# Optimization experiments

Hardware: AMD Instinct MI355X
Metric: run time of the kernel (lower is better)

Reference implementation:

```python
import jax, jax.numpy as jnp
import numpy as np
from jax import lax

# ---- static config (matches init_kwargs) ----
B, D, H, HD, MLP = 64, 768, 12, 64, 3072
DEPTH = 11                     # trunk blocks; block 12 is used (twice) as b1/b2
IMG_H, IMG_W, P, S = 256, 128, 16, 12
NY, NX = (IMG_H - P) // S + 1, (IMG_W - P) // S + 1   # 21, 10
NP = NY * NX                   # 210 patches
N = NP + 1                     # +CLS = 211 tokens
NUM_CIDS = 8
SCALE = HD ** -0.5
SIE = 3.0                      # sie_xishu
SHIFT, GROUPS, DIV = 5, 2, 4
EPS = 1e-6
_PNAMES = ["ln1_g", "ln1_b", "qkv_w", "qkv_b", "proj_w", "proj_b",
           "ln2_g", "ln2_b", "fc1_w", "fc1_b", "fc2_w", "fc2_b"]


def layernorm(x, g, b):
    m = jnp.mean(x, -1, keepdims=True)
    v = jnp.mean(jnp.square(x - m), -1, keepdims=True)
    return (x - m) * lax.rsqrt(v + EPS) * g + b


def block(x, p):
    """Pre-norm ViT block: manual attention (q@k.T softmax @v) + GELU MLP."""
    ln1g, ln1b, qkvw, qkvb, projw, projb, ln2g, ln2b, fc1w, fc1b, fc2w, fc2b = p
    Bn, Nn = x.shape[0], x.shape[1]
    h = layernorm(x, ln1g, ln1b)
    qkv = (h @ qkvw + qkvb).reshape(Bn, Nn, 3, H, HD)
    q, k, v = qkv[:, :, 0], qkv[:, :, 1], qkv[:, :, 2]           # [B,N,H,HD]
    attn = jax.nn.softmax(jnp.einsum('bnhd,bmhd->bhnm', q * SCALE, k), axis=-1)
    o = jnp.einsum('bhnm,bmhd->bnhd', attn, v).reshape(Bn, Nn, D)
    x = x + o @ projw + projb
    h = layernorm(x, ln2g, ln2b)
    return x + jax.nn.gelu(h @ fc1w + fc1b, approximate=False) @ fc2w + fc2b


def _block_params(k, lead=()):
    ks = jax.random.split(k, 4)
    z = lambda s: jnp.zeros(lead + s, jnp.float32)
    o = lambda s: jnp.ones(lead + s, jnp.float32)
    r = lambda kk, s, fan: jax.random.normal(kk, lead + s, jnp.float32) * (fan ** -0.5)
    return dict(ln1_g=o((D,)), ln1_b=z((D,)),
                qkv_w=r(ks[0], (D, 3 * D), D), qkv_b=z((3 * D,)),
                proj_w=r(ks[1], (D, D), D), proj_b=z((D,)),
                ln2_g=o((D,)), ln2_b=z((D,)),
                fc1_w=r(ks[2], (D, MLP), D), fc1_b=z((MLP,)),
                fc2_w=r(ks[3], (MLP, D), MLP), fc2_b=z((D,)))


def setup_inputs() -> dict:
    key = jax.random.key(0)
    k = jax.random.split(key, 8)
    inp = {
        "x": jax.random.normal(k[0], (B, 3, IMG_H, IMG_W), jnp.float32),
        "cids": jax.random.randint(k[1], (B,), 0, NUM_CIDS),
        "conv_w": jax.random.normal(k[2], (D, 3, P, P), jnp.float32) * np.float32(np.sqrt(2.0 / (P * P * D))),
        "conv_b": jnp.zeros((D,), jnp.float32),
        "cls_token": jax.random.normal(k[3], (1, 1, D), jnp.float32) * 0.02,
        "pos_embed": jax.random.normal(k[4], (1, N, D), jnp.float32) * 0.02,
        "sie_embed": jax.random.normal(k[5], (NUM_CIDS, 1, D), jnp.float32) * 0.02,
    }
    for name, arr in _block_params(k[6], (DEPTH,)).items():
        inp["blk_" + name] = arr
    for pre, kk in (("b1_", jax.random.fold_in(key, 101)), ("b2_", jax.random.fold_in(key, 102))):
        for name, arr in _block_params(kk).items():
            inp[pre + name] = arr
        inp[pre + "norm_g"] = jnp.ones((D,), jnp.float32)
        inp[pre + "norm_b"] = jnp.zeros((D,), jnp.float32)
    return inp


def reference(x, cids, conv_w, conv_b, cls_token, pos_embed, sie_embed,
              blk_ln1_g, blk_ln1_b, blk_qkv_w, blk_qkv_b, blk_proj_w, blk_proj_b,
              blk_ln2_g, blk_ln2_b, blk_fc1_w, blk_fc1_b, blk_fc2_w, blk_fc2_b,
              b1_ln1_g, b1_ln1_b, b1_qkv_w, b1_qkv_b, b1_proj_w, b1_proj_b,
              b1_ln2_g, b1_ln2_b, b1_fc1_w, b1_fc1_b, b1_fc2_w, b1_fc2_b,
              b1_norm_g, b1_norm_b,
              b2_ln1_g, b2_ln1_b, b2_qkv_w, b2_qkv_b, b2_proj_w, b2_proj_b,
              b2_ln2_g, b2_ln2_b, b2_fc1_w, b2_fc1_b, b2_fc2_w, b2_fc2_b,
              b2_norm_g, b2_norm_b):
    Bn = x.shape[0]
    # overlapping patch embed: Conv2d(3->768, k=16, s=12), flatten, transpose
    y = lax.conv_general_dilated(x, conv_w, (S, S), 'VALID',
                                 dimension_numbers=('NCHW', 'OIHW', 'NCHW'))
    y = (y + conv_b[None, :, None, None]).reshape(Bn, D, NP).transpose(0, 2, 1)
    t = jnp.concatenate([jnp.broadcast_to(cls_token, (Bn, 1, D)), y], axis=1)
    t = t + pos_embed + SIE * sie_embed[cids]   # SIE camera embedding
    # 11 trunk blocks via scan over stacked params
    stk = (blk_ln1_g, blk_ln1_b, blk_qkv_w, blk_qkv_b, blk_proj_w, blk_proj_b,
           blk_ln2_g, blk_ln2_b, blk_fc1_w, blk_fc1_b, blk_fc2_w, blk_fc2_b)
    t = lax.scan(lambda c, p: (block(c, p), None), t, stk)[0]
    # global branch: b1 = block12 + final norm, take CLS
    b1p = (b1_ln1_g, b1_ln1_b, b1_qkv_w, b1_qkv_b, b1_proj_w, b1_proj_b,
           b1_ln2_g, b1_ln2_b, b1_fc1_w, b1_fc1_b, b1_fc2_w, b1_fc2_b)
    f0 = layernorm(block(t, b1p), b1_norm_g, b1_norm_b)[:, 0]
    # shuffle_unit(t, shift=5, group=2, begin=1) -> jigsaw rearranged patches [B,210,D]
    xs = jnp.concatenate([t[:, SHIFT:], t[:, 1:SHIFT]], axis=1)
    xs = xs.reshape(Bn, GROUPS, -1, D).transpose(0, 2, 1, 3).reshape(Bn, -1, D)
    token = t[:, 0:1]
    pl = NP // DIV                                   # 52
    b2p = (b2_ln1_g, b2_ln1_b, b2_qkv_w, b2_qkv_b, b2_proj_w, b2_proj_b,
           b2_ln2_g, b2_ln2_b, b2_fc1_w, b2_fc1_b, b2_fc2_w, b2_fc2_b)
    feats = [f0]
    for i in range(DIV):
        seg = jnp.concatenate([token, xs[:, i * pl:(i + 1) * pl]], axis=1)   # [B,53,D]
        feats.append(layernorm(block(seg, b2p), b2_norm_g, b2_norm_b)[:, 0])
    # eval output with neck_feat='before': necks pass features through;
    # concat global + local/divide_length -> [B, 5*768]
    return jnp.concatenate([feats[0]] + [f / DIV for f in feats[1:]], axis=1)
```

## Files before the change

kernel.cpp:

```cpp
#include <hip/hip_runtime.h>
#include <hip/hip_bf16.h>
#include <cstdint>
#include <cstddef>
#include <math.h>

using bf16 = __hip_bfloat16;
typedef __bf16 bf16x8 __attribute__((ext_vector_type(8)));
typedef float f32x4 __attribute__((ext_vector_type(4)));

static constexpr int NHEAD = 12;
static constexpr int NTOK  = 211;
static constexpr int DEPTH = 11;

static __device__ __forceinline__ void gload_lds16(const bf16* g, bf16* lds) {
  __builtin_amdgcn_global_load_lds(
      (const __attribute__((address_space(1))) uint32_t*)g,
      (__attribute__((address_space(3))) uint32_t*)lds,
      16, 0, 0);
}

__device__ __forceinline__ float gelu_f(float x) {
  float u = x * (0.7978845608f + 0.0356774081f * x * x);
  float t = 1.f - 2.f / (__expf(2.f * u) + 1.f);
  return 0.5f * x * (1.f + t);
}

static __device__ __forceinline__ unsigned short bf16_bits(float x) {
  return __builtin_bit_cast(unsigned short, __float2bfloat16(x));
}

template <bool GELU, bool RES, typename CT>
__global__ __launch_bounds__(256) void gemm_db(
    const bf16* __restrict__ A, const bf16* __restrict__ Bt,
    const float* __restrict__ bias, const float* __restrict__ res,
    CT* __restrict__ C, int M, int N, int K, int gn, int sA, int sR, int sC)
{
  __shared__ bf16 sb[2][8192];

  const int tid = threadIdx.x;
  const int w = tid >> 6, l = tid & 63;
  const int lr = l & 15, lg = l >> 4;
  const int wr = (w >> 1) * 64, wc = (w & 1) * 64;

  const int nwg = gridDim.x, lin = blockIdx.x;
  const int q = nwg >> 3, r = nwg & 7;
  const int xcd = lin & 7, pos = lin >> 3;
  const int wg = (xcd < r ? xcd * (q + 1) : r * (q + 1) + (xcd - r) * q) + pos;
  const int bm0 = (wg / gn) * 128, bn0 = (wg % gn) * 128;

  f32x4 acc[4][4];
#pragma unroll
  for (int i = 0; i < 4; ++i)
#pragma unroll
    for (int j = 0; j < 4; ++j) acc[i][j] = f32x4{0.f, 0.f, 0.f, 0.f};

  size_t aof[2], bof[2]; int dst[2];
#pragma unroll
  for (int j = 0; j < 2; ++j) {
    const int c = j * 256 + tid;
    const int row = c >> 2;
    const int ch = (c & 3) ^ ((row >> 1) & 3);
    int ar = bm0 + row; if (ar >= M) ar = M - 1;
    aof[j] = (size_t)ar * sA + ch * 8;
    bof[j] = (size_t)(bn0 + row) * K + ch * 8;
    dst[j] = c * 8;
  }

  const int nt = K >> 5;

  auto stage = [&](int t) {
    bf16* s = sb[t & 1];
    const size_t ko = (size_t)t * 32;
    gload_lds16(A + aof[0] + ko, s + dst[0]);
    gload_lds16(A + aof[1] + ko, s + dst[1]);
    gload_lds16(Bt + bof[0] + ko, s + 4096 + dst[0]);
    gload_lds16(Bt + bof[1] + ko, s + 4096 + dst[1]);
  };

  stage(0);
  __syncthreads();

  const int swz = (lg ^ ((lr >> 1) & 3)) * 8;

  for (int t = 0; t < nt; ++t) {
    if (t + 1 < nt) stage(t + 1);
    const bf16* As = sb[t & 1];
    const bf16* Bs = As + 4096;
    bf16x8 af[4], bv[4];
#pragma unroll
    for (int mi = 0; mi < 4; ++mi)
      af[mi] = *(const bf16x8*)(As + (wr + mi * 16 + lr) * 32 + swz);
#pragma unroll
    for (int ni = 0; ni < 4; ++ni)
      bv[ni] = *(const bf16x8*)(Bs + (wc + ni * 16 + lr) * 32 + swz);
#pragma unroll
    for (int mi = 0; mi < 4; ++mi)
#pragma unroll
      for (int ni = 0; ni < 4; ++ni)
        acc[mi][ni] = __builtin_amdgcn_mfma_f32_16x16x32_bf16(af[mi], bv[ni], acc[mi][ni], 0, 0, 0);
    __syncthreads();
  }

  if constexpr (sizeof(CT) == 2) {
    char* lb = (char*)sb;
#pragma unroll
    for (int mi = 0; mi < 4; ++mi) {
#pragma unroll
      for (int ni = 0; ni < 4; ++ni) {
        const int cloc = wc + ni * 16 + lr;
        const float bvl = bias[bn0 + cloc];
#pragma unroll
        for (int r2 = 0; r2 < 4; ++r2) {
          const int rowl = wr + mi * 16 + lg * 4 + r2;
          float v = acc[mi][ni][r2] + bvl;
          if constexpr (GELU) v = gelu_f(v);
          *(unsigned short*)(lb + rowl * 256 + ((cloc * 2) ^ (((rowl >> 1) & 6) << 4))) =
              bf16_bits(v);
        }
      }
    }
    __syncthreads();
#pragma unroll
    for (int j = 0; j < 8; ++j) {
      const int flat = j * 256 + tid;
      const int row = flat >> 4, ch = flat & 15;
      const int grow = bm0 + row;
      if (grow < M) {
        const f32x4 v = *(const f32x4*)(lb + row * 256 + ((ch * 16) ^ (((row >> 1) & 6) << 4)));
        *(f32x4*)((char*)C + ((size_t)grow * sC + bn0 + ch * 8) * 2) = v;
      }
    }
  } else {
#pragma unroll
    for (int mi = 0; mi < 4; ++mi) {
#pragma unroll
      for (int ni = 0; ni < 4; ++ni) {
        const int col = bn0 + wc + ni * 16 + lr;
        const float bvl = bias[col];
#pragma unroll
        for (int r2 = 0; r2 < 4; ++r2) {
          const int row = bm0 + wr + mi * 16 + lg * 4 + r2;
          if (row < M) {
            float v = acc[mi][ni][r2] + bvl;
            if constexpr (GELU) v = gelu_f(v);
            if constexpr (RES) v += res[(size_t)row * sR + col];
            C[(size_t)row * sC + col] = v;
          }
        }
      }
    }
  }
}

__global__ __launch_bounds__(256) void vtrans_kernel(
    const bf16* __restrict__ qkv, bf16* __restrict__ vT, int ntok, int pad)
{
  __shared__ unsigned short t[224 * 65];
  const int bb = blockIdx.x, h = blockIdx.y;
  const unsigned short* src = (const unsigned short*)qkv + (size_t)bb * ntok * 2304 + 1536 + h * 64;
  for (int idx = threadIdx.x; idx < ntok * 64; idx += 256) {
    int tok = idx >> 6, d = idx & 63;
    t[tok * 65 + d] = src[(size_t)tok * 2304 + d];
  }
  __syncthreads();
  unsigned short* dst = (unsigned short*)vT + (size_t)(bb * 12 + h) * 64 * pad;
  for (int idx = threadIdx.x; idx < 64 * ntok; idx += 256) {
    int d = idx / ntok, tok = idx - d * ntok;
    dst[(size_t)d * pad + tok] = t[tok * 65 + d];
  }
}

template <int NKF, bool ONLY0>
__global__ __launch_bounds__(256) void attn_kernel(
    const bf16* __restrict__ qkv, const bf16* __restrict__ vT,
    bf16* __restrict__ ao, int ntok, int pad)
{
  constexpr int NPAD = NKF * 16;
  __shared__ bf16 Pl[4][16][NPAD];
  const int bb = blockIdx.x;
  const int h = blockIdx.y;
  const int tid = threadIdx.x;
  const int w = tid >> 6, l = tid & 63;
  const int lr = l & 15, lg = l >> 4;
  if (ONLY0 && w > 0) return;
  const __bf16* base = reinterpret_cast<const __bf16*>(qkv) + (size_t)bb * ntok * 2304 + h * 64;
  const __bf16* vt = reinterpret_cast<const __bf16*>(vT) + (size_t)(bb * 12 + h) * 64 * pad;

  for (int qt = w; qt < (ONLY0 ? 1 : NKF); qt += 4) {
    int qrow = qt * 16 + lr; if (qrow >= ntok) qrow = ntok - 1;
    const __bf16* qp = base + (size_t)qrow * 2304 + lg * 8;
    const bf16x8 qf0 = *reinterpret_cast<const bf16x8*>(qp);
    const bf16x8 qf1 = *reinterpret_cast<const bf16x8*>(qp + 32);

    f32x4 s[NKF];
#pragma unroll
    for (int kf = 0; kf < NKF; ++kf) {
      int krow = kf * 16 + lr; if (krow >= ntok) krow = ntok - 1;
      const __bf16* kp = base + (size_t)krow * 2304 + 768 + lg * 8;
      f32x4 a = f32x4{0.f, 0.f, 0.f, 0.f};
      a = __builtin_amdgcn_mfma_f32_16x16x32_bf16(qf0, *reinterpret_cast<const bf16x8*>(kp), a, 0, 0, 0);
      a = __builtin_amdgcn_mfma_f32_16x16x32_bf16(qf1, *reinterpret_cast<const bf16x8*>(kp + 32), a, 0, 0, 0);
      s[kf] = a;
    }

    float rs[4];
#pragma unroll
    for (int r = 0; r < 4; ++r) {
      float mx = -1e30f;
#pragma unroll
      for (int kf = 0; kf < NKF; ++kf)
        if (kf * 16 + lr < ntok) mx = fmaxf(mx, s[kf][r]);
#pragma unroll
      for (int d = 1; d < 16; d <<= 1) mx = fmaxf(mx, __shfl_xor(mx, d));
      float sum = 0.f;
#pragma unroll
      for (int kf = 0; kf < NKF; ++kf) {
        float p = 0.f;
        if (kf * 16 + lr < ntok) p = __expf((s[kf][r] - mx) * 0.125f);
        sum += p;
        Pl[w][lg * 4 + r][kf * 16 + lr] = __float2bfloat16(p);
      }
#pragma unroll
      for (int d = 1; d < 16; d <<= 1) sum += __shfl_xor(sum, d);
      rs[r] = sum;
    }
    __builtin_amdgcn_s_waitcnt(0);

    f32x4 o[4];
#pragma unroll
    for (int ni = 0; ni < 4; ++ni) o[ni] = f32x4{0.f, 0.f, 0.f, 0.f};
#pragma unroll
    for (int ks = 0; ks < NPAD / 32; ++ks) {
      const bf16x8 pa = *reinterpret_cast<const bf16x8*>(&Pl[w][lr][ks * 32 + lg * 8]);
#pragma unroll
      for (int ni = 0; ni < 4; ++ni) {
        const bf16x8 vb = *reinterpret_cast<const bf16x8*>(
            vt + (size_t)(ni * 16 + lr) * pad + ks * 32 + lg * 8);
        o[ni] = __builtin_amdgcn_mfma_f32_16x16x32_bf16(pa, vb, o[ni], 0, 0, 0);
      }
    }
#pragma unroll
    for (int ni = 0; ni < 4; ++ni)
#pragma unroll
      for (int r = 0; r < 4; ++r) {
        int qq = qt * 16 + lg * 4 + r;
        if (qq < (ONLY0 ? 1 : ntok)) {
          float val = o[ni][r] / rs[r];
          ao[((size_t)bb * ntok + qq) * 768 + h * 64 + ni * 16 + lr] = __float2bfloat16(val);
        }
      }
  }
}

__global__ __launch_bounds__(256) void ln_kernel(
    const float* __restrict__ x, const float* __restrict__ g, const float* __restrict__ b,
    bf16* __restrict__ out, int Mrows)
{
  int row = blockIdx.x * 4 + (threadIdx.x >> 6);
  if (row >= Mrows) return;
  int l = threadIdx.x & 63;
  const float4* xr = reinterpret_cast<const float4*>(x + (size_t)row * 768);
  float4 v[3]; float s = 0.f;
#pragma unroll
  for (int i = 0; i < 3; ++i) {
    v[i] = xr[l + i * 64];
    s += v[i].x + v[i].y + v[i].z + v[i].w;
  }
#pragma unroll
  for (int d = 1; d < 64; d <<= 1) s += __shfl_xor(s, d);
  float mean = s * (1.f / 768.f);
  float s2 = 0.f;
#pragma unroll
  for (int i = 0; i < 3; ++i) {
    float a0 = v[i].x - mean, a1 = v[i].y - mean, a2 = v[i].z - mean, a3 = v[i].w - mean;
    s2 += a0 * a0 + a1 * a1 + a2 * a2 + a3 * a3;
  }
#pragma unroll
  for (int d = 1; d < 64; d <<= 1) s2 += __shfl_xor(s2, d);
  float rstd = rsqrtf(s2 * (1.f / 768.f) + 1e-6f);
  const float4* g4 = reinterpret_cast<const float4*>(g);
  const float4* b4 = reinterpret_cast<const float4*>(b);
  unsigned short* orow = reinterpret_cast<unsigned short*>(out + (size_t)row * 768);
#pragma unroll
  for (int i = 0; i < 3; ++i) {
    float4 gg = g4[l + i * 64], bb = b4[l + i * 64];
    ushort4 pk;
    pk.x = bf16_bits((v[i].x - mean) * rstd * gg.x + bb.x);
    pk.y = bf16_bits((v[i].y - mean) * rstd * gg.y + bb.y);
    pk.z = bf16_bits((v[i].z - mean) * rstd * gg.z + bb.z);
    pk.w = bf16_bits((v[i].w - mean) * rstd * gg.w + bb.w);
    *reinterpret_cast<ushort4*>(orow + (l + i * 64) * 4) = pk;
  }
}

__global__ __launch_bounds__(256) void ln_head_kernel(
    const float* __restrict__ x, int tokstride, const float* __restrict__ g,
    const float* __restrict__ b, float* __restrict__ out, int nbb, int mode)
{
  int bb = blockIdx.x * 4 + (threadIdx.x >> 6);
  if (bb >= nbb) return;
  int l = threadIdx.x & 63;
  const float* xr = x + (size_t)bb * tokstride * 768;
  float v[12]; float s = 0.f;
#pragma unroll
  for (int i = 0; i < 12; ++i) { v[i] = xr[l + i * 64]; s += v[i]; }
#pragma unroll
  for (int d = 1; d < 64; d <<= 1) s += __shfl_xor(s, d);
  float mean = s * (1.f / 768.f);
  float s2 = 0.f;
#pragma unroll
  for (int i = 0; i < 12; ++i) { float t = v[i] - mean; s2 += t * t; }
#pragma unroll
  for (int d = 1; d < 64; d <<= 1) s2 += __shfl_xor(s2, d);
  float rstd = rsqrtf(s2 * (1.f / 768.f) + 1e-6f);
  float scale = mode ? 0.25f : 1.f;
  int b_ = mode ? (bb & 63) : bb;
  int off = mode ? (1 + (bb >> 6)) * 768 : 0;
  float* orow = out + (size_t)b_ * 3840 + off;
#pragma unroll
  for (int i = 0; i < 12; ++i) {
    orow[l + i * 64] = ((v[i] - mean) * rstd * g[l + i * 64] + b[l + i * 64]) * scale;
  }
}

__global__ __launch_bounds__(256) void transpose4_k(
    const float* __restrict__ w0, const float* __restrict__ w1,
    const float* __restrict__ w2, const float* __restrict__ w3,
    bf16* __restrict__ d0, bf16* __restrict__ d1,
    bf16* __restrict__ d2, bf16* __restrict__ d3)
{
  __shared__ float tile[32][33];
  int id = blockIdx.x;
  const float* in; bf16* out; int R, C, tt;
  if (id < 1728)      { in = w0; out = d0; R = 768;  C = 2304; tt = id; }
  else if (id < 2304) { in = w1; out = d1; R = 768;  C = 768;  tt = id - 1728; }
  else if (id < 4608) { in = w2; out = d2; R = 768;  C = 3072; tt = id - 2304; }
  else                { in = w3; out = d3; R = 3072; C = 768;  tt = id - 4608; }
  const int tc = C >> 5;
  int c0 = (tt % tc) * 32, r0 = (tt / tc) * 32;
  int tx = threadIdx.x & 31, ty = threadIdx.x >> 5;
#pragma unroll
  for (int i = 0; i < 4; ++i) {
    int rr = ty + i * 8;
    tile[rr][tx] = in[(size_t)(r0 + rr) * C + c0 + tx];
  }
  __syncthreads();
#pragma unroll
  for (int i = 0; i < 4; ++i) {
    int c = ty + i * 8;
    out[(size_t)(c0 + c) * R + r0 + tx] = __float2bfloat16(tile[tx][c]);
  }
}

__global__ void cast_kernel(const float* __restrict__ in, bf16* __restrict__ out, int n)
{
  int idx = blockIdx.x * 256 + threadIdx.x;
  if (idx < n) out[idx] = __float2bfloat16(in[idx]);
}

__global__ void im2col_kernel(const float* __restrict__ x, bf16* __restrict__ pm)
{
  int idx = blockIdx.x * 256 + threadIdx.x;
  if (idx >= 13440 * 768) return;
  int k = idx % 768;
  int m = idx / 768;
  int b = m / 210, p = m % 210;
  int py = p / 10, px = p % 10;
  int c = k >> 8, ij = k & 255, i = ij >> 4, j = ij & 15;
  pm[idx] = __float2bfloat16(x[(((size_t)b * 3 + c) * 256 + py * 12 + i) * 128 + px * 12 + j]);
}

__global__ void assemble_kernel(
    const bf16* __restrict__ y, const float* __restrict__ cls, const float* __restrict__ pos,
    const float* __restrict__ sie, const int* __restrict__ cids, float* __restrict__ tA)
{
  int idx = blockIdx.x * 256 + threadIdx.x;
  if (idx >= 13504 * 768) return;
  int d = idx % 768;
  int t = (idx / 768) % 211;
  int b = idx / (768 * 211);
  float v = pos[t * 768 + d] + 3.0f * sie[cids[b] * 768 + d];
  if (t == 0) v += cls[d];
  else v += __bfloat162float(y[((size_t)b * 210 + (t - 1)) * 768 + d]);
  tA[idx] = v;
}

__global__ void gather_kernel(const float* __restrict__ tA, float* __restrict__ tB)
{
  int idx = blockIdx.x * 256 + threadIdx.x;
  if (idx >= 256 * 53 * 768) return;
  int d = idx % 768;
  int jj = (idx / 768) % 53;
  int bb = idx / (768 * 53);
  int i = bb >> 6, b = bb & 63;
  int src;
  if (jj == 0) src = 0;
  else {
    int jx = i * 52 + (jj - 1);
    int mm = (jx & 1) * 105 + (jx >> 1);
    src = (mm < 206) ? (5 + mm) : (1 + (mm - 206));
  }
  tB[idx] = tA[((size_t)b * 211 + src) * 768 + d];
}

struct BlkP {
  const float *ln1_g, *ln1_b, *qkv_w, *qkv_b, *proj_w, *proj_b;
  const float *ln2_g, *ln2_b, *fc1_w, *fc1_b, *fc2_w, *fc2_b;
};

extern "C" void kernel_launch(void* const* d_in, const int* in_sizes, int n_in,
                              void* d_out, int out_size, void* d_ws, size_t ws_size,
                              hipStream_t stream)
{
  (void)in_sizes; (void)n_in; (void)out_size; (void)ws_size;
  const float* xin   = (const float*)d_in[0];
  const int*   cids  = (const int*)  d_in[1];
  const float* convw = (const float*)d_in[2];
  const float* convb = (const float*)d_in[3];
  const float* cls   = (const float*)d_in[4];
  const float* pos   = (const float*)d_in[5];
  const float* sie   = (const float*)d_in[6];
  float* out = (float*)d_out;

  char* ws = (char*)d_ws;
  bf16*  qkvT = (bf16*)(ws + 0);
  bf16*  projT = (bf16*)(ws + 3538944);
  bf16*  fc1T = (bf16*)(ws + 4718592);
  bf16*  fc2T = (bf16*)(ws + 9437184);
  float* tA   = (float*)(ws + 14155776);
  float* tB   = (float*)(ws + 55640064);
  bf16*  hb   = (bf16*)(ws + 97320960);
  bf16*  big  = (bf16*)(ws + 118161408);
  bf16*  ao   = (bf16*)(ws + 201523200);
  bf16*  vTb  = (bf16*)(ws + 222363648);
  char*  sbuf = ws + 118161408 + 73400320;
  float* y0   = (float*)(sbuf);
  bf16*  hb0  = (bf16*)(sbuf + 786432);
  bf16*  big0 = (bf16*)(sbuf + 1179648);
  float* f0b  = (float*)(sbuf + 2752512);

  dim3 blk(256);

  auto apply_block = [&](float* xbuf, const BlkP& p, int nb, int ntok_) {
    const int M = nb * ntok_;
    const int gm = (M + 127) / 128;
    const int pad = (ntok_ == NTOK) ? 224 : 64;
    transpose4_k<<<dim3(6912), blk, 0, stream>>>(
        p.qkv_w, p.proj_w, p.fc1_w, p.fc2_w, qkvT, projT, fc1T, fc2T);
    ln_kernel<<<dim3((M + 3) / 4), blk, 0, stream>>>(xbuf, p.ln1_g, p.ln1_b, hb, M);
    gemm_db<false, false, bf16><<<dim3(gm * 18), blk, 0, stream>>>(
        hb, qkvT, p.qkv_b, nullptr, big, M, 2304, 768, 18, 768, 2304, 2304);
    vtrans_kernel<<<dim3(nb, NHEAD), blk, 0, stream>>>(big, vTb, ntok_, pad);
    attn_kernel<14, false><<<dim3(nb, NHEAD), blk, 0, stream>>>(big, vTb, ao, ntok_, pad);
    gemm_db<false, true, float><<<dim3(gm * 6), blk, 0, stream>>>(
        ao, projT, p.proj_b, xbuf, xbuf, M, 768, 768, 6, 768, 768, 768);
    ln_kernel<<<dim3((M + 3) / 4), blk, 0, stream>>>(xbuf, p.ln2_g, p.ln2_b, hb, M);
    gemm_db<true, false, bf16><<<dim3(gm * 24), blk, 0, stream>>>(
        hb, fc1T, p.fc1_b, nullptr, big, M, 3072, 768, 24, 768, 3072, 3072);
    gemm_db<false, true, float><<<dim3(gm * 6), blk, 0, stream>>>(
        big, fc2T, p.fc2_b, xbuf, xbuf, M, 768, 3072, 6, 3072, 768, 768);
  };

  auto apply_head_block = [&](const float* xsrc, const BlkP& p, int nb, int ntok_,
                              const float* ng, const float* nbias, int mode) {
    const int M = nb * ntok_;
    const int gm = (M + 127) / 128;
    const int gm0 = (nb + 127) / 128;
    const int pad = (ntok_ == NTOK) ? 224 : 64;
    const int ts = ntok_ * 768;
    transpose4_k<<<dim3(6912), blk, 0, stream>>>(
        p.qkv_w, p.proj_w, p.fc1_w, p.fc2_w, qkvT, projT, fc1T, fc2T);
    ln_kernel<<<dim3((M + 3) / 4), blk, 0, stream>>>(xsrc, p.ln1_g, p.ln1_b, hb, M);
    gemm_db<false, false, bf16><<<dim3(gm * 18), blk, 0, stream>>>(
        hb, qkvT, p.qkv_b, nullptr, big, M, 2304, 768, 18, 768, 2304, 2304);
    vtrans_kernel<<<dim3(nb, NHEAD), blk, 0, stream>>>(big, vTb, ntok_, pad);
    if (ntok_ == NTOK)
      attn_kernel<14, true><<<dim3(nb, NHEAD), blk, 0, stream>>>(big, vTb, ao, ntok_, pad);
    else
      attn_kernel<4, true><<<dim3(nb, NHEAD), blk, 0, stream>>>(big, vTb, ao, ntok_, pad);
    gemm_db<false, true, float><<<dim3(gm0 * 6), blk, 0, stream>>>(
        ao, projT, p.proj_b, xsrc, y0, nb, 768, 768, 6, ts, ts, 768);
    ln_kernel<<<dim3((nb + 3) / 4), blk, 0, stream>>>(y0, p.ln2_g, p.ln2_b, hb0, nb);
    gemm_db<true, false, bf16><<<dim3(gm0 * 24), blk, 0, stream>>>(
        hb0, fc1T, p.fc1_b, nullptr, big0, nb, 3072, 768, 24, 768, 3072, 3072);
    gemm_db<false, true, float><<<dim3(gm0 * 6), blk, 0, stream>>>(
        big0, fc2T, p.fc2_b, y0, f0b, nb, 768, 3072, 6, 3072, 768, 768);
    ln_head_kernel<<<dim3((nb + 3) / 4), blk, 0, stream>>>(
        f0b, 1, ng, nbias, out, nb, mode);
  };

  {
    int total = 13440 * 768;
    im2col_kernel<<<dim3((total + 255) / 256), blk, 0, stream>>>(xin, big);
    int nw = 768 * 768;
    cast_kernel<<<dim3((nw + 255) / 256), blk, 0, stream>>>(convw, qkvT, nw);
    gemm_db<false, false, bf16><<<dim3(105 * 6), blk, 0, stream>>>(
        big, qkvT, convb, nullptr, ao, 13440, 768, 768, 6, 768, 768, 768);
    total = 13504 * 768;
    assemble_kernel<<<dim3((total + 255) / 256), blk, 0, stream>>>(ao, cls, pos, sie, cids, tA);
  }

  const float* bp[12];
  for (int i = 0; i < 12; ++i) bp[i] = (const float*)d_in[7 + i];
  for (int dd = 0; dd < DEPTH; ++dd) {
    BlkP p;
    p.ln1_g = bp[0] + dd * 768;                p.ln1_b = bp[1] + dd * 768;
    p.qkv_w = bp[2] + (size_t)dd * 768 * 2304; p.qkv_b = bp[3] + dd * 2304;
    p.proj_w = bp[4] + (size_t)dd * 768 * 768; p.proj_b = bp[5] + dd * 768;
    p.ln2_g = bp[6] + dd * 768;                p.ln2_b = bp[7] + dd * 768;
    p.fc1_w = bp[8] + (size_t)dd * 768 * 3072; p.fc1_b = bp[9] + dd * 3072;
    p.fc2_w = bp[10] + (size_t)dd * 3072 * 768; p.fc2_b = bp[11] + dd * 768;
    apply_block(tA, p, 64, NTOK);
  }

  {
    BlkP p;
    p.ln1_g = (const float*)d_in[19]; p.ln1_b = (const float*)d_in[20];
    p.qkv_w = (const float*)d_in[21]; p.qkv_b = (const float*)d_in[22];
    p.proj_w = (const float*)d_in[23]; p.proj_b = (const float*)d_in[24];
    p.ln2_g = (const float*)d_in[25]; p.ln2_b = (const float*)d_in[26];
    p.fc1_w = (const float*)d_in[27]; p.fc1_b = (const float*)d_in[28];
    p.fc2_w = (const float*)d_in[29]; p.fc2_b = (const float*)d_in[30];
    apply_head_block(tA, p, 64, NTOK,
                     (const float*)d_in[31], (const float*)d_in[32], 0);
  }

  {
    int total = 256 * 53 * 768;
    gather_kernel<<<dim3((total + 255) / 256), blk, 0, stream>>>(tA, tB);
    BlkP p;
    p.ln1_g = (const float*)d_in[33]; p.ln1_b = (const float*)d_in[34];
    p.qkv_w = (const float*)d_in[35]; p.qkv_b = (const float*)d_in[36];
    p.proj_w = (const float*)d_in[37]; p.proj_b = (const float*)d_in[38];
    p.ln2_g = (const float*)d_in[39]; p.ln2_b = (const float*)d_in[40];
    p.fc1_w = (const float*)d_in[41]; p.fc1_b = (const float*)d_in[42];
    p.fc2_w = (const float*)d_in[43]; p.fc2_b = (const float*)d_in[44];
    apply_head_block(tB, p, 256, 53,
                     (const float*)d_in[45], (const float*)d_in[46], 1);
  }
}
```

Baseline: 5.167 ms.

## Switch GEMM to 32x32 MFMA, fuse LN with weight transpose, trim head QKV

```diff
diff --git a/kernel.cpp b/kernel.cpp
--- a/kernel.cpp
+++ b/kernel.cpp
@@ -7,6 +7,7 @@
 using bf16 = __hip_bfloat16;
 typedef __bf16 bf16x8 __attribute__((ext_vector_type(8)));
 typedef float f32x4 __attribute__((ext_vector_type(4)));
+typedef float f32x16 __attribute__((ext_vector_type(16)));
 
 static constexpr int NHEAD = 12;
 static constexpr int NTOK  = 211;
@@ -39,7 +40,7 @@
 
   const int tid = threadIdx.x;
   const int w = tid >> 6, l = tid & 63;
-  const int lr = l & 15, lg = l >> 4;
+  const int l31 = l & 31, lh = l >> 5;
   const int wr = (w >> 1) * 64, wc = (w & 1) * 64;
 
   const int nwg = gridDim.x, lin = blockIdx.x;
@@ -48,11 +49,13 @@
   const int wg = (xcd < r ? xcd * (q + 1) : r * (q + 1) + (xcd - r) * q) + pos;
   const int bm0 = (wg / gn) * 128, bn0 = (wg % gn) * 128;
 
-  f32x4 acc[4][4];
-#pragma unroll
-  for (int i = 0; i < 4; ++i)
-#pragma unroll
-    for (int j = 0; j < 4; ++j) acc[i][j] = f32x4{0.f, 0.f, 0.f, 0.f};
+  f32x16 acc[2][2];
+#pragma unroll
+  for (int i = 0; i < 2; ++i)
+#pragma unroll
+    for (int j = 0; j < 2; ++j)
+#pragma unroll
+      for (int e = 0; e < 16; ++e) acc[i][j][e] = 0.f;
 
   size_t aof[2], bof[2]; int dst[2];
 #pragma unroll
@@ -80,38 +83,50 @@
   stage(0);
   __syncthreads();
 
-  const int swz = (lg ^ ((lr >> 1) & 3)) * 8;
+  const int cswz0 = ((lh)     ^ ((l31 >> 1) & 3)) * 8;
+  const int cswz1 = ((2 + lh) ^ ((l31 >> 1) & 3)) * 8;
 
   for (int t = 0; t < nt; ++t) {
     if (t + 1 < nt) stage(t + 1);
     const bf16* As = sb[t & 1];
     const bf16* Bs = As + 4096;
-    bf16x8 af[4], bv[4];
-#pragma unroll
-    for (int mi = 0; mi < 4; ++mi)
-      af[mi] = *(const bf16x8*)(As + (wr + mi * 16 + lr) * 32 + swz);
-#pragma unroll
-    for (int ni = 0; ni < 4; ++ni)
-      bv[ni] = *(const bf16x8*)(Bs + (wc + ni * 16 + lr) * 32 + swz);
-#pragma unroll
-    for (int mi = 0; mi < 4; ++mi)
-#pragma unroll
-      for (int ni = 0; ni < 4; ++ni)
-        acc[mi][ni] = __builtin_amdgcn_mfma_f32_16x16x32_bf16(af[mi], bv[ni], acc[mi][ni], 0, 0, 0);
+    bf16x8 af[2][2], bv[2][2];
+#pragma unroll
+    for (int mi = 0; mi < 2; ++mi) {
+      const int arow = (wr + mi * 32 + l31) * 32;
+      af[mi][0] = *(const bf16x8*)(As + arow + cswz0);
+      af[mi][1] = *(const bf16x8*)(As + arow + cswz1);
+    }
+#pragma unroll
+    for (int ni = 0; ni < 2; ++ni) {
+      const int brow = (wc + ni * 32 + l31) * 32;
+      bv[ni][0] = *(const bf16x8*)(Bs + brow + cswz0);
+      bv[ni][1] = *(const bf16x8*)(Bs + brow + cswz1);
+    }
+#pragma unroll
+    for (int mi = 0; mi < 2; ++mi)
+#pragma unroll
+      for (int ni = 0; ni < 2; ++ni)
+        acc[mi][ni] = __builtin_amdgcn_mfma_f32_32x32x16_bf16(af[mi][0], bv[ni][0], acc[mi][ni], 0, 0, 0);
+#pragma unroll
+    for (int mi = 0; mi < 2; ++mi)
+#pragma unroll
+      for (int ni = 0; ni < 2; ++ni)
+        acc[mi][ni] = __builtin_amdgcn_mfma_f32_32x32x16_bf16(af[mi][1], bv[ni][1], acc[mi][ni], 0, 0, 0);
     __syncthreads();
   }
 
   if constexpr (sizeof(CT) == 2) {
     char* lb = (char*)sb;
 #pragma unroll
-    for (int mi = 0; mi < 4; ++mi) {
-#pragma unroll
-      for (int ni = 0; ni < 4; ++ni) {
-        const int cloc = wc + ni * 16 + lr;
+    for (int mi = 0; mi < 2; ++mi) {
+#pragma unroll
+      for (int ni = 0; ni < 2; ++ni) {
+        const int cloc = wc + ni * 32 + l31;
         const float bvl = bias[bn0 + cloc];
 #pragma unroll
-        for (int r2 = 0; r2 < 4; ++r2) {
-          const int rowl = wr + mi * 16 + lg * 4 + r2;
+        for (int r2 = 0; r2 < 16; ++r2) {
+          const int rowl = wr + mi * 32 + (r2 & 3) + 8 * (r2 >> 2) + 4 * lh;
           float v = acc[mi][ni][r2] + bvl;
           if constexpr (GELU) v = gelu_f(v);
           *(unsigned short*)(lb + rowl * 256 + ((cloc * 2) ^ (((rowl >> 1) & 6) << 4))) =
@@ -132,14 +147,14 @@
     }
   } else {
 #pragma unroll
-    for (int mi = 0; mi < 4; ++mi) {
-#pragma unroll
-      for (int ni = 0; ni < 4; ++ni) {
-        const int col = bn0 + wc + ni * 16 + lr;
+    for (int mi = 0; mi < 2; ++mi) {
+#pragma unroll
+      for (int ni = 0; ni < 2; ++ni) {
+        const int col = bn0 + wc + ni * 32 + l31;
         const float bvl = bias[col];
 #pragma unroll
-        for (int r2 = 0; r2 < 4; ++r2) {
-          const int row = bm0 + wr + mi * 16 + lg * 4 + r2;
+        for (int r2 = 0; r2 < 16; ++r2) {
+          const int row = bm0 + wr + mi * 32 + (r2 & 3) + 8 * (r2 >> 2) + 4 * lh;
           if (row < M) {
             float v = acc[mi][ni][r2] + bvl;
             if constexpr (GELU) v = gelu_f(v);
@@ -252,13 +267,10 @@
   }
 }
 
-__global__ __launch_bounds__(256) void ln_kernel(
+static __device__ __forceinline__ void ln_row(
     const float* __restrict__ x, const float* __restrict__ g, const float* __restrict__ b,
-    bf16* __restrict__ out, int Mrows)
-{
-  int row = blockIdx.x * 4 + (threadIdx.x >> 6);
-  if (row >= Mrows) return;
-  int l = threadIdx.x & 63;
+    bf16* __restrict__ out, int row, int l)
+{
   const float4* xr = reinterpret_cast<const float4*>(x + (size_t)row * 768);
   float4 v[3]; float s = 0.f;
 #pragma unroll
@@ -293,44 +305,30 @@
   }
 }
 
-__global__ __launch_bounds__(256) void ln_head_kernel(
-    const float* __restrict__ x, int tokstride, const float* __restrict__ g,
-    const float* __restrict__ b, float* __restrict__ out, int nbb, int mode)
-{
-  int bb = blockIdx.x * 4 + (threadIdx.x >> 6);
-  if (bb >= nbb) return;
-  int l = threadIdx.x & 63;
-  const float* xr = x + (size_t)bb * tokstride * 768;
-  float v[12]; float s = 0.f;
-#pragma unroll
-  for (int i = 0; i < 12; ++i) { v[i] = xr[l + i * 64]; s += v[i]; }
-#pragma unroll
-  for (int d = 1; d < 64; d <<= 1) s += __shfl_xor(s, d);
-  float mean = s * (1.f / 768.f);
-  float s2 = 0.f;
-#pragma unroll
-  for (int i = 0; i < 12; ++i) { float t = v[i] - mean; s2 += t * t; }
-#pragma unroll
-  for (int d = 1; d < 64; d <<= 1) s2 += __shfl_xor(s2, d);
-  float rstd = rsqrtf(s2 * (1.f / 768.f) + 1e-6f);
-  float scale = mode ? 0.25f : 1.f;
-  int b_ = mode ? (bb & 63) : bb;
-  int off = mode ? (1 + (bb >> 6)) * 768 : 0;
-  float* orow = out + (size_t)b_ * 3840 + off;
-#pragma unroll
-  for (int i = 0; i < 12; ++i) {
-    orow[l + i * 64] = ((v[i] - mean) * rstd * g[l + i * 64] + b[l + i * 64]) * scale;
-  }
-}
-
-__global__ __launch_bounds__(256) void transpose4_k(
+__global__ __launch_bounds__(256) void ln_kernel(
+    const float* __restrict__ x, const float* __restrict__ g, const float* __restrict__ b,
+    bf16* __restrict__ out, int Mrows)
+{
+  int row = blockIdx.x * 4 + (threadIdx.x >> 6);
+  if (row >= Mrows) return;
+  ln_row(x, g, b, out, row, threadIdx.x & 63);
+}
+
+__global__ __launch_bounds__(256) void tln_kernel(
     const float* __restrict__ w0, const float* __restrict__ w1,
     const float* __restrict__ w2, const float* __restrict__ w3,
     bf16* __restrict__ d0, bf16* __restrict__ d1,
-    bf16* __restrict__ d2, bf16* __restrict__ d3)
+    bf16* __restrict__ d2, bf16* __restrict__ d3,
+    const float* __restrict__ x, const float* __restrict__ g,
+    const float* __restrict__ b, bf16* __restrict__ outh, int Mrows)
 {
   __shared__ float tile[32][33];
   int id = blockIdx.x;
+  if (id >= 6912) {
+    int row = (id - 6912) * 4 + (threadIdx.x >> 6);
+    if (row < Mrows) ln_row(x, g, b, outh, row, threadIdx.x & 63);
+    return;
+  }
   const float* in; bf16* out; int R, C, tt;
   if (id < 1728)      { in = w0; out = d0; R = 768;  C = 2304; tt = id; }
   else if (id < 2304) { in = w1; out = d1; R = 768;  C = 768;  tt = id - 1728; }
@@ -352,22 +350,51 @@
   }
 }
 
-__global__ void cast_kernel(const float* __restrict__ in, bf16* __restrict__ out, int n)
+__global__ __launch_bounds__(256) void ln_head_kernel(
+    const float* __restrict__ x, int tokstride, const float* __restrict__ g,
+    const float* __restrict__ b, float* __restrict__ out, int nbb, int mode)
+{
+  int bb = blockIdx.x * 4 + (threadIdx.x >> 6);
+  if (bb >= nbb) return;
+  int l = threadIdx.x & 63;
+  const float* xr = x + (size_t)bb * tokstride * 768;
+  float v[12]; float s = 0.f;
+#pragma unroll
+  for (int i = 0; i < 12; ++i) { v[i] = xr[l + i * 64]; s += v[i]; }
+#pragma unroll
+  for (int d = 1; d < 64; d <<= 1) s += __shfl_xor(s, d);
+  float mean = s * (1.f / 768.f);
+  float s2 = 0.f;
+#pragma unroll
+  for (int i = 0; i < 12; ++i) { float t = v[i] - mean; s2 += t * t; }
+#pragma unroll
+  for (int d = 1; d < 64; d <<= 1) s2 += __shfl_xor(s2, d);
+  float rstd = rsqrtf(s2 * (1.f / 768.f) + 1e-6f);
+  float scale = mode ? 0.25f : 1.f;
+  int b_ = mode ? (bb & 63) : bb;
+  int off = mode ? (1 + (bb >> 6)) * 768 : 0;
+  float* orow = out + (size_t)b_ * 3840 + off;
+#pragma unroll
+  for (int i = 0; i < 12; ++i) {
+    orow[l + i * 64] = ((v[i] - mean) * rstd * g[l + i * 64] + b[l + i * 64]) * scale;
+  }
+}
+
+__global__ void prep_kernel(const float* __restrict__ x, bf16* __restrict__ pm,
+                            const float* __restrict__ convw, bf16* __restrict__ cw)
 {
   int idx = blockIdx.x * 256 + threadIdx.x;
-  if (idx < n) out[idx] = __float2bfloat16(in[idx]);
-}
-
-__global__ void im2col_kernel(const float* __restrict__ x, bf16* __restrict__ pm)
-{
-  int idx = blockIdx.x * 256 + threadIdx.x;
-  if (idx >= 13440 * 768) return;
-  int k = idx % 768;
-  int m = idx / 768;
-  int b = m / 210, p = m % 210;
-  int py = p / 10, px = p % 10;
-  int c = k >> 8, ij = k & 255, i = ij >> 4, j = ij & 15;
-  pm[idx] = __float2bfloat16(x[(((size_t)b * 3 + c) * 256 + py * 12 + i) * 128 + px * 12 + j]);
+  if (idx < 13440 * 768) {
+    int k = idx % 768;
+    int m = idx / 768;
+    int b = m / 210, p = m % 210;
+    int py = p / 10, px = p % 10;
+    int c = k >> 8, ij = k & 255, i = ij >> 4, j = ij & 15;
+    pm[idx] = __float2bfloat16(x[(((size_t)b * 3 + c) * 256 + py * 12 + i) * 128 + px * 12 + j]);
+  } else {
+    int idx2 = idx - 13440 * 768;
+    if (idx2 < 768 * 768) cw[idx2] = __float2bfloat16(convw[idx2]);
+  }
 }
 
 __global__ void assemble_kernel(
@@ -445,9 +472,9 @@
     const int M = nb * ntok_;
     const int gm = (M + 127) / 128;
     const int pad = (ntok_ == NTOK) ? 224 : 64;
-    transpose4_k<<<dim3(6912), blk, 0, stream>>>(
-        p.qkv_w, p.proj_w, p.fc1_w, p.fc2_w, qkvT, projT, fc1T, fc2T);
-    ln_kernel<<<dim3((M + 3) / 4), blk, 0, stream>>>(xbuf, p.ln1_g, p.ln1_b, hb, M);
+    tln_kernel<<<dim3(6912 + (M + 3) / 4), blk, 0, stream>>>(
+        p.qkv_w, p.proj_w, p.fc1_w, p.fc2_w, qkvT, projT, fc1T, fc2T,
+        xbuf, p.ln1_g, p.ln1_b, hb, M);
     gemm_db<false, false, bf16><<<dim3(gm * 18), blk, 0, stream>>>(
         hb, qkvT, p.qkv_b, nullptr, big, M, 2304, 768, 18, 768, 2304, 2304);
     vtrans_kernel<<<dim3(nb, NHEAD), blk, 0, stream>>>(big, vTb, ntok_, pad);
@@ -468,11 +495,15 @@
     const int gm0 = (nb + 127) / 128;
     const int pad = (ntok_ == NTOK) ? 224 : 64;
     const int ts = ntok_ * 768;
-    transpose4_k<<<dim3(6912), blk, 0, stream>>>(
-        p.qkv_w, p.proj_w, p.fc1_w, p.fc2_w, qkvT, projT, fc1T, fc2T);
-    ln_kernel<<<dim3((M + 3) / 4), blk, 0, stream>>>(xsrc, p.ln1_g, p.ln1_b, hb, M);
-    gemm_db<false, false, bf16><<<dim3(gm * 18), blk, 0, stream>>>(
-        hb, qkvT, p.qkv_b, nullptr, big, M, 2304, 768, 18, 768, 2304, 2304);
+    tln_kernel<<<dim3(6912 + (M + 3) / 4), blk, 0, stream>>>(
+        p.qkv_w, p.proj_w, p.fc1_w, p.fc2_w, qkvT, projT, fc1T, fc2T,
+        xsrc, p.ln1_g, p.ln1_b, hb, M);
+    gemm_db<false, false, bf16><<<dim3(gm * 12), blk, 0, stream>>>(
+        hb, qkvT + 768 * 768, p.qkv_b + 768, nullptr, big + 768,
+        M, 1536, 768, 12, 768, 0, 2304);
+    gemm_db<false, false, bf16><<<dim3(gm0 * 6), blk, 0, stream>>>(
+        hb, qkvT, p.qkv_b, nullptr, big,
+        nb, 768, 768, 6, ntok_ * 768, 0, ntok_ * 2304);
     vtrans_kernel<<<dim3(nb, NHEAD), blk, 0, stream>>>(big, vTb, ntok_, pad);
     if (ntok_ == NTOK)
       attn_kernel<14, true><<<dim3(nb, NHEAD), blk, 0, stream>>>(big, vTb, ao, ntok_, pad);
@@ -490,10 +521,8 @@
   };
 
   {
-    int total = 13440 * 768;
-    im2col_kernel<<<dim3((total + 255) / 256), blk, 0, stream>>>(xin, big);
-    int nw = 768 * 768;
-    cast_kernel<<<dim3((nw + 255) / 256), blk, 0, stream>>>(convw, qkvT, nw);
+    int total = 13440 * 768 + 768 * 768;
+    prep_kernel<<<dim3((total + 255) / 256), blk, 0, stream>>>(xin, big, convw, qkvT);
     gemm_db<false, false, bf16><<<dim3(105 * 6), blk, 0, stream>>>(
         big, qkvT, convb, nullptr, ao, 13440, 768, 768, 6, 768, 768, 768);
     total = 13504 * 768;
```

Result: slower. 5.390 ms (+4.3%).
